# Performance work log

Measured on AMD Instinct MI355X. Metric: run time of the kernel, lower is better.

The kernel has to match this reference:

```python
import jax, jax.numpy as jnp
import numpy as np

T, H, I, E, TOPK = 1024, 1024, 2048, 8, 2


def setup_inputs() -> dict:
    key = jax.random.key(0)
    k1, k2, k3, k4, k5, k6 = jax.random.split(key, 6)
    hidden_states = jax.random.normal(k1, (T, H), dtype=jnp.float32)
    expert_affinities = jax.random.uniform(k2, (T, E), dtype=jnp.float32)
    expert_index = jax.random.randint(k3, (T, TOPK), 0, E, dtype=jnp.int64)
    # Expert GLU MLP weights: gate/up [E,H,I], down [E,I,H]
    w_gate = jax.random.normal(k4, (E, H, I), dtype=jnp.float32) / np.sqrt(H)
    w_up = jax.random.normal(k5, (E, H, I), dtype=jnp.float32) / np.sqrt(H)
    w_down = jax.random.normal(k6, (E, I, H), dtype=jnp.float32) / np.sqrt(I)
    return {
        "hidden_states": hidden_states,
        "expert_affinities": expert_affinities,
        "expert_index": expert_index,
        "w_gate": w_gate,
        "w_up": w_up,
        "w_down": w_down,
        "seq_len": T,
    }


def reference(hidden_states, expert_affinities, expert_index, w_gate, w_up, w_down, seq_len):
    # Gather top-k affinities and renormalize (normalize_top_k_affinities=True)
    topk_aff = jnp.take_along_axis(expert_affinities, expert_index, axis=1)  # [T,K]
    topk_aff = topk_aff / jnp.sum(topk_aff, axis=1, keepdims=True)
    # Dense combine weights [T,E] (scatter of normalized top-k affinities)
    t_idx = jnp.arange(hidden_states.shape[0])[:, None]
    combine = jnp.zeros((hidden_states.shape[0], w_gate.shape[0]),
                        dtype=hidden_states.dtype).at[t_idx, expert_index].add(topk_aff)
    # GLU expert MLP for all experts (E small, grouped-GEMM form)
    g = jnp.einsum("th,ehi->tei", hidden_states, w_gate)  # [T,E,I]
    u = jnp.einsum("th,ehi->tei", hidden_states, w_up)    # [T,E,I]
    act = jax.nn.silu(g) * u                               # [T,E,I]
    # Down-projection fused with affinity-weighted combine
    out = jnp.einsum("tei,eih,te->th", act, w_down, combine)  # [T,H]
    return out
```

## Files before the change

kernel.cpp:

```cpp
#include <hip/hip_runtime.h>
#include <hip/hip_bf16.h>
#include <math.h>

#define T_ 1024
#define H_ 1024
#define I_ 2048
#define E_ 8
#define NSLOT 2048

#define BM 128
#define BK 32
#define BN1 64
#define BN2 64
#define NCHUNK_CAP 24
#define SPLITK2 2

typedef __attribute__((ext_vector_type(8))) short bf16x8;
typedef __attribute__((ext_vector_type(4))) float f32x4;
typedef __attribute__((ext_vector_type(4))) unsigned uint4v;
typedef __attribute__((ext_vector_type(2))) unsigned uint2v;

#define MFMA_BF16 __builtin_amdgcn_mfma_f32_16x16x32_bf16

__device__ __forceinline__ short f2bf(float f) {
  union { float f; unsigned u; } v; v.f = f;
  unsigned r = v.u + 0x7FFFu + ((v.u >> 16) & 1u);
  return (short)(r >> 16);
}
__device__ __forceinline__ unsigned cvtpk(float lo, float hi) {
  unsigned r;
  asm("v_cvt_pk_bf16_f32 %0, %1, %2" : "=v"(r) : "v"(lo), "v"(hi));
  return r;
}
__device__ __forceinline__ void gll16(const void* g, void* l) {
  __builtin_amdgcn_global_load_lds(
      (const __attribute__((address_space(1))) void*)g,
      (__attribute__((address_space(3))) void*)l, 16, 0, 0);
}

__device__ __forceinline__ void pipe_barrier6() {
  __builtin_amdgcn_sched_barrier(0);
  asm volatile("s_waitcnt vmcnt(6) lgkmcnt(0)" ::: "memory");
  __builtin_amdgcn_s_barrier();
  __builtin_amdgcn_sched_barrier(0);
}
__device__ __forceinline__ void pipe_barrier4() {
  __builtin_amdgcn_sched_barrier(0);
  asm volatile("s_waitcnt vmcnt(4) lgkmcnt(0)" ::: "memory");
  __builtin_amdgcn_s_barrier();
  __builtin_amdgcn_sched_barrier(0);
}
__device__ __forceinline__ void drain_barrier() {
  __builtin_amdgcn_sched_barrier(0);
  asm volatile("s_waitcnt vmcnt(0) lgkmcnt(0)" ::: "memory");
  __builtin_amdgcn_s_barrier();
  __builtin_amdgcn_sched_barrier(0);
}

__device__ __forceinline__ int rswz(int row) { return (row >> 1) & 3; }
__device__ __forceinline__ unsigned tile_addr(int row, int g) {
  return (unsigned)(row * 64 + (((g ^ rswz(row)) & 3) << 4));
}

__global__ __launch_bounds__(256) void k_prep(const float* __restrict__ hs,
                                              short* __restrict__ hs_bf) {
  int i = (blockIdx.x * 256 + threadIdx.x) * 8;
  float4 v0 = *(const float4*)&hs[i];
  float4 v1 = *(const float4*)&hs[i + 4];
  uint4v p;
  p.x = cvtpk(v0.x, v0.y); p.y = cvtpk(v0.z, v0.w);
  p.z = cvtpk(v1.x, v1.y); p.w = cvtpk(v1.z, v1.w);
  *(uint4v*)&hs_bf[i] = p;
}

__global__ __launch_bounds__(1024) void k_build(
    const float* __restrict__ aff, const int* __restrict__ eidx,
    int* __restrict__ meta, int* __restrict__ slot_tok, float* __restrict__ slot_w) {
  __shared__ int cnt[E_];
  __shared__ int soff[E_ + 1];
  int t = threadIdx.x;
  if (t < E_) cnt[t] = 0;
  __syncthreads();
  int e0 = eidx[t * 2 + 0];
  int e1 = eidx[t * 2 + 1];
  float a0 = aff[t * E_ + e0];
  float a1 = aff[t * E_ + e1];
  float inv = 1.0f / (a0 + a1);
  int r0 = atomicAdd(&cnt[e0], 1);
  int r1 = atomicAdd(&cnt[e1], 1);
  __syncthreads();
  if (t == 0) {
    int s = 0;
    for (int e = 0; e < E_; ++e) { soff[e] = s; s += cnt[e]; }
    soff[E_] = s;
    int nc = 0;
    for (int e = 0; e < E_; ++e)
      for (int c = soff[e]; c < soff[e] + cnt[e]; c += BM)
        meta[16 + nc++] = e | (c << 8);
    meta[9] = nc;
  }
  __syncthreads();
  if (t <= E_) meta[t] = soff[t];
  int s0 = soff[e0] + r0;
  int s1 = soff[e1] + r1;
  slot_tok[s0] = t; slot_w[s0] = a0 * inv;
  slot_tok[s1] = t; slot_w[s1] = a1 * inv;
}

__global__ __launch_bounds__(256, 2) void k_gemm1(
    const short* __restrict__ hs_bf, const float* __restrict__ wg,
    const float* __restrict__ wu, const int* __restrict__ meta,
    const int* __restrict__ slot_tok, short* __restrict__ act) {
  int nch = meta[9];
  if (blockIdx.y >= nch) return;
  int ck = meta[16 + blockIdx.y];
  int e = ck & 255;
  int row0 = ck >> 8;
  int rows = min(BM, meta[1 + e] - row0);
  int i0 = blockIdx.x * BN1;

  __shared__ short sA[4][BM * BK];
  __shared__ short sB[2][2][BN1 * BK];

  int tid = threadIdx.x;
  int lane = tid & 63;
  int w = tid >> 6;
  int wm = w >> 1, wn = w & 1;
  int lr = lane & 15;
  int g = lane >> 4;

  const float* wgE = wg + (size_t)e * H_ * I_;
  const float* wuE = wu + (size_t)e * H_ * I_;

  int r_a0 = 32 * w + (lane >> 2);
  int r_a1 = r_a0 + 16;
  int tok0 = slot_tok[row0 + min(r_a0, rows - 1)];
  int tok1 = slot_tok[row0 + min(r_a1, rows - 1)];
  const short* srcA0 = hs_bf + (size_t)tok0 * H_ + ((((lane & 3) ^ rswz(r_a0)) & 3) << 3);
  const short* srcA1 = hs_bf + (size_t)tok1 * H_ + ((((lane & 3) ^ rswz(r_a1)) & 3) << 3);

  int mat = tid >> 7;
  int kq = (tid >> 4) & 7;
  int nq = tid & 15;
  const float* srcB = (mat ? wuE : wgE) + (size_t)(4 * kq) * I_ + i0 + 4 * nq;

  f32x4 accg[4][2], accu[4][2];
#pragma unroll
  for (int mf = 0; mf < 4; ++mf)
#pragma unroll
    for (int nf = 0; nf < 2; ++nf) {
      accg[mf][nf] = (f32x4){0.f, 0.f, 0.f, 0.f};
      accu[mf][nf] = (f32x4){0.f, 0.f, 0.f, 0.f};
    }

  f32x4 bs0[4], bs1[4];

  const int NT = H_ / BK;

  gll16(srcA0, &sA[0][(32 * w) * 32]);
  gll16(srcA1, &sA[0][(32 * w + 16) * 32]);
#pragma unroll
  for (int j = 0; j < 4; ++j) bs0[j] = *(const f32x4*)(srcB + (size_t)j * I_);
  gll16(srcA0 + BK, &sA[1][(32 * w) * 32]);
  gll16(srcA1 + BK, &sA[1][(32 * w + 16) * 32]);
#pragma unroll
  for (int j = 0; j < 4; ++j) bs1[j] = *(const f32x4*)(srcB + (size_t)(BK + j) * I_);
  {
    char* dst = (char*)&sB[0][mat][0];
#pragma unroll
    for (int c = 0; c < 4; ++c) {
      int n = 4 * nq + c;
      uint2v wv;
      wv.x = cvtpk(bs0[0][c], bs0[1][c]);
      wv.y = cvtpk(bs0[2][c], bs0[3][c]);
      *(uint2v*)(dst + tile_addr(n, kq >> 1) + ((kq & 1) << 3)) = wv;
    }
  }
  drain_barrier();

#define G1_ITER(U, bsL, bsC) do {                                              \
    int t_ = base + (U);                                                       \
    const char* curA = (const char*)&sA[t_ & 3][0];                            \
    if (t_ + 2 < NT) {                                                         \
      short* nxtA = &sA[(t_ + 2) & 3][0];                                      \
      gll16(srcA0 + (size_t)(t_ + 2) * BK, nxtA + (32 * w) * 32);              \
      gll16(srcA1 + (size_t)(t_ + 2) * BK, nxtA + (32 * w + 16) * 32);         \
      const float* sb = srcB + (size_t)(t_ + 2) * BK * I_;                     \
      bsL[0] = *(const f32x4*)(sb);                                            \
      bsL[1] = *(const f32x4*)(sb + I_);                                       \
      bsL[2] = *(const f32x4*)(sb + 2 * I_);                                   \
      bsL[3] = *(const f32x4*)(sb + 3 * I_);                                   \
    }                                                                          \
    bf16x8 a0 = *(const bf16x8*)(curA + tile_addr(wm * 64 + lr, g));           \
    bf16x8 a1 = *(const bf16x8*)(curA + tile_addr(wm * 64 + 16 + lr, g));      \
    bf16x8 a2 = *(const bf16x8*)(curA + tile_addr(wm * 64 + 32 + lr, g));      \
    bf16x8 a3 = *(const bf16x8*)(curA + tile_addr(wm * 64 + 48 + lr, g));      \
    const char* pg = (const char*)&sB[(U)][0][0];                              \
    const char* pu = (const char*)&sB[(U)][1][0];                              \
    unsigned ob0 = tile_addr(wn * 32 + lr, g);                                 \
    unsigned ob1 = tile_addr(wn * 32 + 16 + lr, g);                            \
    bf16x8 g0 = *(const bf16x8*)(pg + ob0);                                    \
    bf16x8 g1 = *(const bf16x8*)(pg + ob1);                                    \
    bf16x8 u0 = *(const bf16x8*)(pu + ob0);                                    \
    bf16x8 u1 = *(const bf16x8*)(pu + ob1);                                    \
    accg[0][0] = MFMA_BF16(a0, g0, accg[0][0], 0, 0, 0);                       \
    accg[0][1] = MFMA_BF16(a0, g1, accg[0][1], 0, 0, 0);                       \
    accg[1][0] = MFMA_BF16(a1, g0, accg[1][0], 0, 0, 0);                       \
    accg[1][1] = MFMA_BF16(a1, g1, accg[1][1], 0, 0, 0);                       \
    accg[2][0] = MFMA_BF16(a2, g0, accg[2][0], 0, 0, 0);                       \
    accg[2][1] = MFMA_BF16(a2, g1, accg[2][1], 0, 0, 0);                       \
    accg[3][0] = MFMA_BF16(a3, g0, accg[3][0], 0, 0, 0);                       \
    accg[3][1] = MFMA_BF16(a3, g1, accg[3][1], 0, 0, 0);                       \
    accu[0][0] = MFMA_BF16(a0, u0, accu[0][0], 0, 0, 0);                       \
    accu[0][1] = MFMA_BF16(a0, u1, accu[0][1], 0, 0, 0);                       \
    accu[1][0] = MFMA_BF16(a1, u0, accu[1][0], 0, 0, 0);                       \
    accu[1][1] = MFMA_BF16(a1, u1, accu[1][1], 0, 0, 0);                       \
    accu[2][0] = MFMA_BF16(a2, u0, accu[2][0], 0, 0, 0);                       \
    accu[2][1] = MFMA_BF16(a2, u1, accu[2][1], 0, 0, 0);                       \
    accu[3][0] = MFMA_BF16(a3, u0, accu[3][0], 0, 0, 0);                       \
    accu[3][1] = MFMA_BF16(a3, u1, accu[3][1], 0, 0, 0);                       \
    if (t_ + 1 < NT) {                                                         \
      char* dst = (char*)&sB[(U) ^ 1][mat][0];                                 \
      _Pragma("unroll")                                                        \
      for (int c = 0; c < 4; ++c) {                                            \
        int n = 4 * nq + c;                                                    \
        uint2v wv;                                                             \
        wv.x = cvtpk(bsC[0][c], bsC[1][c]);                                    \
        wv.y = cvtpk(bsC[2][c], bsC[3][c]);                                    \
        *(uint2v*)(dst + tile_addr(n, kq >> 1) + ((kq & 1) << 3)) = wv;        \
      }                                                                        \
    }                                                                          \
    pipe_barrier6();                                                           \
  } while (0)

  for (int base = 0; base < NT; base += 2) {
    G1_ITER(0, bs0, bs1);
    G1_ITER(1, bs1, bs0);
  }
#undef G1_ITER

#pragma unroll
  for (int mf = 0; mf < 4; ++mf) {
#pragma unroll
    for (int r = 0; r < 4; ++r) {
      int m = wm * 64 + mf * 16 + g * 4 + r;
      if (m < rows) {
#pragma unroll
        for (int nf = 0; nf < 2; ++nf) {
          float gv = accg[mf][nf][r];
          float uv = accu[mf][nf][r];
          float sg = 1.0f / (1.0f + __expf(-gv));
          act[(size_t)(row0 + m) * I_ + i0 + wn * 32 + nf * 16 + lr] = f2bf(gv * sg * uv);
        }
      }
    }
  }
}

__global__ __launch_bounds__(256, 2) void k_gemm2(
    const short* __restrict__ act, const float* __restrict__ wd,
    const int* __restrict__ meta, const int* __restrict__ slot_tok,
    const float* __restrict__ slot_w, float* __restrict__ out) {
  int nch = meta[9];
  if (blockIdx.y >= nch) return;
  int ck = meta[16 + blockIdx.y];
  int e = ck & 255;
  int row0 = ck >> 8;
  int rows = min(BM, meta[1 + e] - row0);
  int h0 = blockIdx.x * BN2;
  int kbase = blockIdx.z * (I_ / SPLITK2);

  __shared__ short sA[4][BM * BK];
  __shared__ short sB[2][BN2 * BK];

  int tid = threadIdx.x;
  int lane = tid & 63;
  int w = tid >> 6;
  int wm = w >> 1, wn = w & 1;
  int lr = lane & 15;
  int g = lane >> 4;

  const float* wdE = wd + (size_t)e * I_ * H_;

  int isB = (w < 2);
  int kq = (tid >> 4) & 7;
  int nq = tid & 15;
  const float* srcB = wdE + (size_t)(kbase + 4 * kq) * H_ + h0 + 4 * nq;
  int wp = w & 1;
  int r_a = 64 * wp + (lane >> 2);
  const short* srcA[4];
#pragma unroll
  for (int p = 0; p < 4; ++p) {
    int rr = r_a + 16 * p;
    int gs = ((lane & 3) ^ rswz(rr)) & 3;
    srcA[p] = act + (size_t)(row0 + min(rr, rows - 1)) * I_ + kbase + (gs << 3);
  }

  f32x4 acc[4][2];
#pragma unroll
  for (int mf = 0; mf < 4; ++mf)
#pragma unroll
    for (int nf = 0; nf < 2; ++nf)
      acc[mf][nf] = (f32x4){0.f, 0.f, 0.f, 0.f};

  f32x4 bs0[4], bs1[4];

  const int NT = (I_ / SPLITK2) / BK;

  if (isB) {
#pragma unroll
    for (int j = 0; j < 4; ++j) bs0[j] = *(const f32x4*)(srcB + (size_t)j * H_);
#pragma unroll
    for (int j = 0; j < 4; ++j) bs1[j] = *(const f32x4*)(srcB + (size_t)(BK + j) * H_);
  } else {
#pragma unroll
    for (int p = 0; p < 4; ++p)
      gll16(srcA[p], &sA[0][(64 * wp + 16 * p) * 32]);
#pragma unroll
    for (int p = 0; p < 4; ++p)
      gll16(srcA[p] + BK, &sA[1][(64 * wp + 16 * p) * 32]);
  }
  if (isB) {
    char* dst = (char*)&sB[0][0];
#pragma unroll
    for (int c = 0; c < 4; ++c) {
      int n = 4 * nq + c;
      uint2v wv;
      wv.x = cvtpk(bs0[0][c], bs0[1][c]);
      wv.y = cvtpk(bs0[2][c], bs0[3][c]);
      *(uint2v*)(dst + tile_addr(n, kq >> 1) + ((kq & 1) << 3)) = wv;
    }
  }
  drain_barrier();

#define G2_ITER(U, bsL, bsC) do {                                              \
    int t_ = base + (U);                                                       \
    const char* curA = (const char*)&sA[t_ & 3][0];                            \
    if (t_ + 2 < NT) {                                                         \
      if (isB) {                                                               \
        const float* sb = srcB + (size_t)(t_ + 2) * BK * H_;                   \
        bsL[0] = *(const f32x4*)(sb);                                          \
        bsL[1] = *(const f32x4*)(sb + H_);                                     \
        bsL[2] = *(const f32x4*)(sb + 2 * H_);                                 \
        bsL[3] = *(const f32x4*)(sb + 3 * H_);                                 \
      } else {                                                                 \
        short* nxtA = &sA[(t_ + 2) & 3][0];                                    \
        gll16(srcA[0] + (size_t)(t_ + 2) * BK, nxtA + (64 * wp) * 32);         \
        gll16(srcA[1] + (size_t)(t_ + 2) * BK, nxtA + (64 * wp + 16) * 32);    \
        gll16(srcA[2] + (size_t)(t_ + 2) * BK, nxtA + (64 * wp + 32) * 32);    \
        gll16(srcA[3] + (size_t)(t_ + 2) * BK, nxtA + (64 * wp + 48) * 32);    \
      }                                                                        \
    }                                                                          \
    bf16x8 a0 = *(const bf16x8*)(curA + tile_addr(wm * 64 + lr, g));           \
    bf16x8 a1 = *(const bf16x8*)(curA + tile_addr(wm * 64 + 16 + lr, g));      \
    bf16x8 a2 = *(const bf16x8*)(curA + tile_addr(wm * 64 + 32 + lr, g));      \
    bf16x8 a3 = *(const bf16x8*)(curA + tile_addr(wm * 64 + 48 + lr, g));      \
    const char* pb = (const char*)&sB[(U)][0];                                 \
    bf16x8 b0 = *(const bf16x8*)(pb + tile_addr(wn * 32 + lr, g));             \
    bf16x8 b1 = *(const bf16x8*)(pb + tile_addr(wn * 32 + 16 + lr, g));        \
    acc[0][0] = MFMA_BF16(a0, b0, acc[0][0], 0, 0, 0);                         \
    acc[0][1] = MFMA_BF16(a0, b1, acc[0][1], 0, 0, 0);                         \
    acc[1][0] = MFMA_BF16(a1, b0, acc[1][0], 0, 0, 0);                         \
    acc[1][1] = MFMA_BF16(a1, b1, acc[1][1], 0, 0, 0);                         \
    acc[2][0] = MFMA_BF16(a2, b0, acc[2][0], 0, 0, 0);                         \
    acc[2][1] = MFMA_BF16(a2, b1, acc[2][1], 0, 0, 0);                         \
    acc[3][0] = MFMA_BF16(a3, b0, acc[3][0], 0, 0, 0);                         \
    acc[3][1] = MFMA_BF16(a3, b1, acc[3][1], 0, 0, 0);                         \
    if (isB && t_ + 1 < NT) {                                                  \
      char* dst = (char*)&sB[(U) ^ 1][0];                                      \
      _Pragma("unroll")                                                        \
      for (int c = 0; c < 4; ++c) {                                            \
        int n = 4 * nq + c;                                                    \
        uint2v wv;                                                             \
        wv.x = cvtpk(bsC[0][c], bsC[1][c]);                                    \
        wv.y = cvtpk(bsC[2][c], bsC[3][c]);                                    \
        *(uint2v*)(dst + tile_addr(n, kq >> 1) + ((kq & 1) << 3)) = wv;        \
      }                                                                        \
    }                                                                          \
    pipe_barrier4();                                                           \
  } while (0)

  for (int base = 0; base < NT; base += 2) {
    G2_ITER(0, bs0, bs1);
    G2_ITER(1, bs1, bs0);
  }
#undef G2_ITER

#pragma unroll
  for (int mf = 0; mf < 4; ++mf) {
#pragma unroll
    for (int r = 0; r < 4; ++r) {
      int m = wm * 64 + mf * 16 + g * 4 + r;
      if (m < rows) {
        int gs = row0 + m;
        float wc = slot_w[gs];
        int tok = slot_tok[gs];
#pragma unroll
        for (int nf = 0; nf < 2; ++nf)
          atomicAdd(&out[(size_t)tok * H_ + h0 + wn * 32 + nf * 16 + lr],
                    acc[mf][nf][r] * wc);
      }
    }
  }
}

extern "C" void kernel_launch(void* const* d_in, const int* in_sizes, int n_in,
                              void* d_out, int out_size, void* d_ws, size_t ws_size,
                              hipStream_t stream) {
  const float* hs   = (const float*)d_in[0];
  const float* aff  = (const float*)d_in[1];
  const int*   eidx = (const int*)d_in[2];
  const float* wg   = (const float*)d_in[3];
  const float* wu   = (const float*)d_in[4];
  const float* wd   = (const float*)d_in[5];
  float* out = (float*)d_out;

  char* ws = (char*)d_ws;
  int*   meta     = (int*)ws;
  int*   slot_tok = (int*)(ws + 256);
  float* slot_w   = (float*)(ws + 256 + NSLOT * 4);
  short* hs_bf    = (short*)(ws + 256 + NSLOT * 8);
  short* act      = (short*)(ws + 256 + NSLOT * 8 + (size_t)T_ * H_ * 2);

  hipMemsetAsync(d_out, 0, (size_t)out_size * sizeof(float), stream);
  k_build<<<1, T_, 0, stream>>>(aff, eidx, meta, slot_tok, slot_w);
  k_prep<<<(T_ * H_) / (256 * 8), 256, 0, stream>>>(hs, hs_bf);
  k_gemm1<<<dim3(I_ / BN1, NCHUNK_CAP), 256, 0, stream>>>(hs_bf, wg, wu, meta, slot_tok, act);
  k_gemm2<<<dim3(H_ / BN2, NCHUNK_CAP, SPLITK2), 256, 0, stream>>>(act, wd, meta, slot_tok, slot_w, out);
}
```

Measured before the change: 103.1 us.

## Fuse prep and build kernels, restructure gemm2 to 512 threads with deeper pipeline

```diff
diff --git a/kernel.cpp b/kernel.cpp
--- a/kernel.cpp
+++ b/kernel.cpp
@@ -44,12 +44,6 @@
   __builtin_amdgcn_s_barrier();
   __builtin_amdgcn_sched_barrier(0);
 }
-__device__ __forceinline__ void pipe_barrier4() {
-  __builtin_amdgcn_sched_barrier(0);
-  asm volatile("s_waitcnt vmcnt(4) lgkmcnt(0)" ::: "memory");
-  __builtin_amdgcn_s_barrier();
-  __builtin_amdgcn_sched_barrier(0);
-}
 __device__ __forceinline__ void drain_barrier() {
   __builtin_amdgcn_sched_barrier(0);
   asm volatile("s_waitcnt vmcnt(0) lgkmcnt(0)" ::: "memory");
@@ -57,13 +51,18 @@
   __builtin_amdgcn_sched_barrier(0);
 }
 
+__device__ __forceinline__ unsigned bswz(int n, int kbyte) {
+  return (unsigned)(n * 64 + (kbyte ^ (((n >> 2) & 3) << 4)));
+}
 __device__ __forceinline__ int rswz(int row) { return (row >> 1) & 3; }
 __device__ __forceinline__ unsigned tile_addr(int row, int g) {
   return (unsigned)(row * 64 + (((g ^ rswz(row)) & 3) << 4));
 }
 
-__global__ __launch_bounds__(256) void k_prep(const float* __restrict__ hs,
-                                              short* __restrict__ hs_bf) {
+__global__ __launch_bounds__(256) void k_prep_build(
+    const float* __restrict__ hs, short* __restrict__ hs_bf,
+    const float* __restrict__ aff, const int* __restrict__ eidx,
+    int* __restrict__ meta, int* __restrict__ slot_tok, float* __restrict__ slot_w) {
   int i = (blockIdx.x * 256 + threadIdx.x) * 8;
   float4 v0 = *(const float4*)&hs[i];
   float4 v1 = *(const float4*)&hs[i + 4];
@@ -71,23 +70,28 @@
   p.x = cvtpk(v0.x, v0.y); p.y = cvtpk(v0.z, v0.w);
   p.z = cvtpk(v1.x, v1.y); p.w = cvtpk(v1.z, v1.w);
   *(uint4v*)&hs_bf[i] = p;
-}
-
-__global__ __launch_bounds__(1024) void k_build(
-    const float* __restrict__ aff, const int* __restrict__ eidx,
-    int* __restrict__ meta, int* __restrict__ slot_tok, float* __restrict__ slot_w) {
+
+  if (blockIdx.x != 0) return;
   __shared__ int cnt[E_];
   __shared__ int soff[E_ + 1];
   int t = threadIdx.x;
   if (t < E_) cnt[t] = 0;
   __syncthreads();
-  int e0 = eidx[t * 2 + 0];
-  int e1 = eidx[t * 2 + 1];
-  float a0 = aff[t * E_ + e0];
-  float a1 = aff[t * E_ + e1];
-  float inv = 1.0f / (a0 + a1);
-  int r0 = atomicAdd(&cnt[e0], 1);
-  int r1 = atomicAdd(&cnt[e1], 1);
+  int e0a[4], e1a[4], r0a[4], r1a[4];
+  float w0a[4], w1a[4];
+#pragma unroll
+  for (int j = 0; j < 4; ++j) {
+    int tok = t + 256 * j;
+    int e0 = eidx[tok * 2 + 0];
+    int e1 = eidx[tok * 2 + 1];
+    float a0 = aff[tok * E_ + e0];
+    float a1 = aff[tok * E_ + e1];
+    float inv = 1.0f / (a0 + a1);
+    r0a[j] = atomicAdd(&cnt[e0], 1);
+    r1a[j] = atomicAdd(&cnt[e1], 1);
+    e0a[j] = e0; e1a[j] = e1;
+    w0a[j] = a0 * inv; w1a[j] = a1 * inv;
+  }
   __syncthreads();
   if (t == 0) {
     int s = 0;
@@ -101,13 +105,17 @@
   }
   __syncthreads();
   if (t <= E_) meta[t] = soff[t];
-  int s0 = soff[e0] + r0;
-  int s1 = soff[e1] + r1;
-  slot_tok[s0] = t; slot_w[s0] = a0 * inv;
-  slot_tok[s1] = t; slot_w[s1] = a1 * inv;
-}
-
-__global__ __launch_bounds__(256, 2) void k_gemm1(
+#pragma unroll
+  for (int j = 0; j < 4; ++j) {
+    int tok = t + 256 * j;
+    int s0 = soff[e0a[j]] + r0a[j];
+    int s1 = soff[e1a[j]] + r1a[j];
+    slot_tok[s0] = tok; slot_w[s0] = w0a[j];
+    slot_tok[s1] = tok; slot_w[s1] = w1a[j];
+  }
+}
+
+__global__ __launch_bounds__(256, 3) void k_gemm1(
     const short* __restrict__ hs_bf, const float* __restrict__ wg,
     const float* __restrict__ wu, const int* __restrict__ meta,
     const int* __restrict__ slot_tok, short* __restrict__ act) {
@@ -257,7 +265,7 @@
   }
 }
 
-__global__ __launch_bounds__(256, 2) void k_gemm2(
+__global__ __launch_bounds__(512, 4) void k_gemm2(
     const short* __restrict__ act, const float* __restrict__ wd,
     const int* __restrict__ meta, const int* __restrict__ slot_tok,
     const float* __restrict__ slot_w, float* __restrict__ out) {
@@ -278,127 +286,86 @@
   int w = tid >> 6;
   int wm = w >> 1, wn = w & 1;
   int lr = lane & 15;
-  int g = lane >> 4;
+  int lk = (lane >> 4) * 8;
 
   const float* wdE = wd + (size_t)e * I_ * H_;
 
-  int isB = (w < 2);
-  int kq = (tid >> 4) & 7;
-  int nq = tid & 15;
-  const float* srcB = wdE + (size_t)(kbase + 4 * kq) * H_ + h0 + 4 * nq;
-  int wp = w & 1;
-  int r_a = 64 * wp + (lane >> 2);
-  const short* srcA[4];
-#pragma unroll
-  for (int p = 0; p < 4; ++p) {
-    int rr = r_a + 16 * p;
-    int gs = ((lane & 3) ^ rswz(rr)) & 3;
-    srcA[p] = act + (size_t)(row0 + min(rr, rows - 1)) * I_ + kbase + (gs << 3);
-  }
-
-  f32x4 acc[4][2];
-#pragma unroll
-  for (int mf = 0; mf < 4; ++mf)
-#pragma unroll
-    for (int nf = 0; nf < 2; ++nf)
-      acc[mf][nf] = (f32x4){0.f, 0.f, 0.f, 0.f};
-
-  f32x4 bs0[4], bs1[4];
+  int ra = min(16 * w + (lane >> 2), rows - 1);
+  const short* srcA = act + (size_t)(row0 + ra) * I_ + kbase + (lane & 3) * 8;
+  int up = tid >> 5;
+  int n2 = (tid & 31) * 2;
+  const float* srcB = wdE + (size_t)(kbase + 2 * up) * H_ + h0 + n2;
+
+  f32x4 acc[2][2];
+#pragma unroll
+  for (int mr = 0; mr < 2; ++mr)
+#pragma unroll
+    for (int nr = 0; nr < 2; ++nr)
+      acc[mr][nr] = (f32x4){0.f, 0.f, 0.f, 0.f};
+
+  float2 bs[4][2];
+
+#pragma unroll
+  for (int p = 0; p < 3; ++p) {
+    gll16(srcA + p * BK, &sA[p][w * 512]);
+    bs[p][0] = *(const float2*)(srcB + (size_t)(p * BK) * H_);
+    bs[p][1] = *(const float2*)(srcB + (size_t)(p * BK + 1) * H_);
+  }
+  *(unsigned*)((char*)&sB[0][0] + bswz(n2, 4 * up))     = cvtpk(bs[0][0].x, bs[0][1].x);
+  *(unsigned*)((char*)&sB[0][0] + bswz(n2 + 1, 4 * up)) = cvtpk(bs[0][0].y, bs[0][1].y);
+  drain_barrier();
 
   const int NT = (I_ / SPLITK2) / BK;
 
-  if (isB) {
-#pragma unroll
-    for (int j = 0; j < 4; ++j) bs0[j] = *(const f32x4*)(srcB + (size_t)j * H_);
-#pragma unroll
-    for (int j = 0; j < 4; ++j) bs1[j] = *(const f32x4*)(srcB + (size_t)(BK + j) * H_);
-  } else {
-#pragma unroll
-    for (int p = 0; p < 4; ++p)
-      gll16(srcA[p], &sA[0][(64 * wp + 16 * p) * 32]);
-#pragma unroll
-    for (int p = 0; p < 4; ++p)
-      gll16(srcA[p] + BK, &sA[1][(64 * wp + 16 * p) * 32]);
-  }
-  if (isB) {
-    char* dst = (char*)&sB[0][0];
-#pragma unroll
-    for (int c = 0; c < 4; ++c) {
-      int n = 4 * nq + c;
-      uint2v wv;
-      wv.x = cvtpk(bs0[0][c], bs0[1][c]);
-      wv.y = cvtpk(bs0[2][c], bs0[3][c]);
-      *(uint2v*)(dst + tile_addr(n, kq >> 1) + ((kq & 1) << 3)) = wv;
-    }
-  }
-  drain_barrier();
-
-#define G2_ITER(U, bsL, bsC) do {                                              \
-    int t_ = base + (U);                                                       \
-    const char* curA = (const char*)&sA[t_ & 3][0];                            \
-    if (t_ + 2 < NT) {                                                         \
-      if (isB) {                                                               \
-        const float* sb = srcB + (size_t)(t_ + 2) * BK * H_;                   \
-        bsL[0] = *(const f32x4*)(sb);                                          \
-        bsL[1] = *(const f32x4*)(sb + H_);                                     \
-        bsL[2] = *(const f32x4*)(sb + 2 * H_);                                 \
-        bsL[3] = *(const f32x4*)(sb + 3 * H_);                                 \
-      } else {                                                                 \
-        short* nxtA = &sA[(t_ + 2) & 3][0];                                    \
-        gll16(srcA[0] + (size_t)(t_ + 2) * BK, nxtA + (64 * wp) * 32);         \
-        gll16(srcA[1] + (size_t)(t_ + 2) * BK, nxtA + (64 * wp + 16) * 32);    \
-        gll16(srcA[2] + (size_t)(t_ + 2) * BK, nxtA + (64 * wp + 32) * 32);    \
-        gll16(srcA[3] + (size_t)(t_ + 2) * BK, nxtA + (64 * wp + 48) * 32);    \
-      }                                                                        \
+#define G2_ITER(U, base_) do {                                                 \
+    int t_ = (base_) + (U);                                                    \
+    if (t_ + 3 < NT) {                                                         \
+      int k3 = (t_ + 3) * BK;                                                  \
+      gll16(srcA + k3, &sA[((U) + 3) & 3][w * 512]);                           \
+      bs[((U) + 3) & 3][0] = *(const float2*)(srcB + (size_t)k3 * H_);         \
+      bs[((U) + 3) & 3][1] = *(const float2*)(srcB + (size_t)(k3 + 1) * H_);   \
     }                                                                          \
-    bf16x8 a0 = *(const bf16x8*)(curA + tile_addr(wm * 64 + lr, g));           \
-    bf16x8 a1 = *(const bf16x8*)(curA + tile_addr(wm * 64 + 16 + lr, g));      \
-    bf16x8 a2 = *(const bf16x8*)(curA + tile_addr(wm * 64 + 32 + lr, g));      \
-    bf16x8 a3 = *(const bf16x8*)(curA + tile_addr(wm * 64 + 48 + lr, g));      \
-    const char* pb = (const char*)&sB[(U)][0];                                 \
-    bf16x8 b0 = *(const bf16x8*)(pb + tile_addr(wn * 32 + lr, g));             \
-    bf16x8 b1 = *(const bf16x8*)(pb + tile_addr(wn * 32 + 16 + lr, g));        \
+    bf16x8 a0 = *(const bf16x8*)&sA[(U)][(wm * 32 + lr) * BK + lk];            \
+    bf16x8 a1 = *(const bf16x8*)&sA[(U)][(wm * 32 + 16 + lr) * BK + lk];       \
+    bf16x8 b0 = *(const bf16x8*)((const char*)&sB[(U) & 1][0]                  \
+                                 + bswz(wn * 32 + lr, lk * 2));                \
+    bf16x8 b1 = *(const bf16x8*)((const char*)&sB[(U) & 1][0]                  \
+                                 + bswz(wn * 32 + 16 + lr, lk * 2));           \
     acc[0][0] = MFMA_BF16(a0, b0, acc[0][0], 0, 0, 0);                         \
     acc[0][1] = MFMA_BF16(a0, b1, acc[0][1], 0, 0, 0);                         \
     acc[1][0] = MFMA_BF16(a1, b0, acc[1][0], 0, 0, 0);                         \
     acc[1][1] = MFMA_BF16(a1, b1, acc[1][1], 0, 0, 0);                         \
-    acc[2][0] = MFMA_BF16(a2, b0, acc[2][0], 0, 0, 0);                         \
-    acc[2][1] = MFMA_BF16(a2, b1, acc[2][1], 0, 0, 0);                         \
-    acc[3][0] = MFMA_BF16(a3, b0, acc[3][0], 0, 0, 0);                         \
-    acc[3][1] = MFMA_BF16(a3, b1, acc[3][1], 0, 0, 0);                         \
-    if (isB && t_ + 1 < NT) {                                                  \
-      char* dst = (char*)&sB[(U) ^ 1][0];                                      \
-      _Pragma("unroll")                                                        \
-      for (int c = 0; c < 4; ++c) {                                            \
-        int n = 4 * nq + c;                                                    \
-        uint2v wv;                                                             \
-        wv.x = cvtpk(bsC[0][c], bsC[1][c]);                                    \
-        wv.y = cvtpk(bsC[2][c], bsC[3][c]);                                    \
-        *(uint2v*)(dst + tile_addr(n, kq >> 1) + ((kq & 1) << 3)) = wv;        \
-      }                                                                        \
+    if (t_ + 1 < NT) {                                                         \
+      int s_ = ((U) + 1) & 3;                                                  \
+      *(unsigned*)((char*)&sB[((U) + 1) & 1][0] + bswz(n2, 4 * up))            \
+          = cvtpk(bs[s_][0].x, bs[s_][1].x);                                   \
+      *(unsigned*)((char*)&sB[((U) + 1) & 1][0] + bswz(n2 + 1, 4 * up))        \
+          = cvtpk(bs[s_][0].y, bs[s_][1].y);                                   \
     }                                                                          \
-    pipe_barrier4();                                                           \
+    pipe_barrier6();                                                           \
   } while (0)
 
-  for (int base = 0; base < NT; base += 2) {
-    G2_ITER(0, bs0, bs1);
-    G2_ITER(1, bs1, bs0);
+  for (int base = 0; base < NT; base += 4) {
+    G2_ITER(0, base);
+    G2_ITER(1, base);
+    G2_ITER(2, base);
+    G2_ITER(3, base);
   }
 #undef G2_ITER
 
 #pragma unroll
-  for (int mf = 0; mf < 4; ++mf) {
+  for (int mr = 0; mr < 2; ++mr) {
 #pragma unroll
     for (int r = 0; r < 4; ++r) {
-      int m = wm * 64 + mf * 16 + g * 4 + r;
+      int m = wm * 32 + mr * 16 + (lane >> 4) * 4 + r;
       if (m < rows) {
         int gs = row0 + m;
         float wc = slot_w[gs];
         int tok = slot_tok[gs];
 #pragma unroll
-        for (int nf = 0; nf < 2; ++nf)
-          atomicAdd(&out[(size_t)tok * H_ + h0 + wn * 32 + nf * 16 + lr],
-                    acc[mf][nf][r] * wc);
+        for (int nr = 0; nr < 2; ++nr)
+          atomicAdd(&out[(size_t)tok * H_ + h0 + wn * 32 + nr * 16 + lr],
+                    acc[mr][nr][r] * wc);
       }
     }
   }
@@ -423,8 +390,10 @@
   short* act      = (short*)(ws + 256 + NSLOT * 8 + (size_t)T_ * H_ * 2);
 
   hipMemsetAsync(d_out, 0, (size_t)out_size * sizeof(float), stream);
-  k_build<<<1, T_, 0, stream>>>(aff, eidx, meta, slot_tok, slot_w);
-  k_prep<<<(T_ * H_) / (256 * 8), 256, 0, stream>>>(hs, hs_bf);
-  k_gemm1<<<dim3(I_ / BN1, NCHUNK_CAP), 256, 0, stream>>>(hs_bf, wg, wu, meta, slot_tok, act);
-  k_gemm2<<<dim3(H_ / BN2, NCHUNK_CAP, SPLITK2), 256, 0, stream>>>(act, wd, meta, slot_tok, slot_w, out);
-}
+  k_prep_build<<<(T_ * H_) / (256 * 8), 256, 0, stream>>>(
+      hs, hs_bf, aff, eidx, meta, slot_tok, slot_w);
+  k_gemm1<<<dim3(I_ / BN1, NCHUNK_CAP), 256, 0, stream>>>(
+      hs_bf, wg, wu, meta, slot_tok, act);
+  k_gemm2<<<dim3(H_ / BN2, NCHUNK_CAP, SPLITK2), 512, 0, stream>>>(
+      act, wd, meta, slot_tok, slot_w, out);
+}
```

Measured after the change: 101.5 us, median of 3. About the same (-1.6%).
